# Optimization experiments

Measured on AMD Instinct MI355X. Metric: run time of the kernel, lower is better.

The kernel has to match this reference:

```python
import jax, jax.numpy as jnp
import numpy as np

R_SOFTPLUS_0 = 1.442695041  # 1/softplus(0) = 1/ln(2)
NEG_INF = -1e9


def setup_inputs() -> dict:
    key = jax.random.key(0)
    ks = jax.random.split(key, 6)
    B, L, E, H = 16, 1024, 512, 8
    Dh = E // H
    return {
        "x": jax.random.normal(ks[0], (B, L, E), jnp.float32),
        "in_proj_weight": jax.random.normal(ks[1], (3 * E, E), jnp.float32) * (E ** -0.5),
        "in_proj_bias": jax.random.normal(ks[2], (3 * E,), jnp.float32) * 0.02,
        "out_proj_weight": jax.random.normal(ks[3], (E, E), jnp.float32) * (E ** -0.5),
        "out_proj_bias": jax.random.normal(ks[4], (E,), jnp.float32) * 0.02,
        "qs_scale": jnp.zeros((Dh,), jnp.float32),  # init.zeros in QueryScaler
        "key_padding_mask": jnp.zeros((B, L), jnp.bool_),  # True = ignore key
    }


def reference(x, in_proj_weight, in_proj_bias, out_proj_weight, out_proj_bias,
              qs_scale, key_padding_mask):
    B, L, E = x.shape
    Dh = qs_scale.shape[0]
    H = E // Dh
    # packed in-projection: q,k,v = x @ W^T + b, split along last dim
    qkv = jnp.einsum("ble,fe->blf", x, in_proj_weight) + in_proj_bias
    q, k, v = jnp.split(qkv, 3, axis=-1)
    q = q.reshape(B, L, H, Dh)
    k = k.reshape(B, L, H, Dh)
    v = v.reshape(B, L, H, Dh)
    # QueryScaler: per-head-dim learned softplus scale on projected q
    q = q * (R_SOFTPLUS_0 * jax.nn.softplus(qs_scale))
    # scaled dot-product attention
    scores = jnp.einsum("blhd,bshd->bhls", q, k) / jnp.sqrt(jnp.asarray(Dh, q.dtype))
    scores = jnp.where(key_padding_mask[:, None, None, :], NEG_INF, scores)
    probs = jax.nn.softmax(scores, axis=-1)
    out = jnp.einsum("bhls,bshd->blhd", probs, v).reshape(B, L, E)
    # output projection
    return jnp.einsum("ble,fe->blf", out, out_proj_weight) + out_proj_bias
```

## Files before the change

### kernel.cpp

```cpp
#include <hip/hip_runtime.h>
#include <hip/hip_bf16.h>
#include <math.h>

#define B_ 16
#define L_ 1024
#define E_ 512
#define H_ 8
#define DH 64

typedef unsigned short u16;
typedef __attribute__((ext_vector_type(8))) short bf16x8;
typedef __attribute__((ext_vector_type(8))) unsigned short u16x8;
typedef __attribute__((ext_vector_type(4))) float f32x4;
typedef __attribute__((ext_vector_type(16))) float f32x16;

#define MFMA16(A, B, C) __builtin_amdgcn_mfma_f32_16x16x32_bf16(A, B, C, 0, 0, 0)
#define MFMA32(A, B, C) __builtin_amdgcn_mfma_f32_32x32x16_bf16(A, B, C, 0, 0, 0)

#if __has_builtin(__builtin_amdgcn_exp2f)
#define EXP2(x) __builtin_amdgcn_exp2f(x)
#else
#define EXP2(x) exp2f(x)
#endif

__device__ inline u16 f2b(float x) {
    __hip_bfloat16 h = __float2bfloat16(x);
    u16 u; __builtin_memcpy(&u, &h, 2); return u;
}

__device__ inline unsigned int cvt_pk_bf16(float a, float b) {
    unsigned int r;
    asm("v_cvt_pk_bf16_f32 %0, %1, %2" : "=v"(r) : "v"(a), "v"(b));
    return r;
}

__global__ void qscale_kernel(const float* __restrict__ qs_scale,
                              float* __restrict__ qscale) {
    int d = threadIdx.x;
    if (d < DH) {
        float x = qs_scale[d];
        float sp = (x > 20.f) ? x : log1pf(expf(x));
        qscale[d] = 1.442695041f * sp * 0.125f * 1.442695041f;
    }
}

__global__ __launch_bounds__(256) void cvt_bf16(
    const float* __restrict__ x, const float* __restrict__ wi,
    const float* __restrict__ wo, u16* __restrict__ xb,
    u16* __restrict__ wib, u16* __restrict__ wob)
{
    int i = blockIdx.x * 256 + threadIdx.x;
    const float* src; u16* dst; size_t off;
    if (i < 1048576)      { src = x;  dst = xb;  off = (size_t)i * 8; }
    else if (i < 1146880) { src = wi; dst = wib; off = (size_t)(i - 1048576) * 8; }
    else                  { src = wo; dst = wob; off = (size_t)(i - 1146880) * 8; }
    float4 a = *(const float4*)(src + off);
    float4 b = *(const float4*)(src + off + 4);
    u16x8 r;
    r[0] = f2b(a.x); r[1] = f2b(a.y); r[2] = f2b(a.z); r[3] = f2b(a.w);
    r[4] = f2b(b.x); r[5] = f2b(b.y); r[6] = f2b(b.z); r[7] = f2b(b.w);
    *(u16x8*)(dst + off) = r;
}

template<int MODE>
__global__ __launch_bounds__(256) void gemm_bf16(
    const u16* __restrict__ A, const u16* __restrict__ W,
    const float* __restrict__ bias, const float* __restrict__ qscale,
    float* __restrict__ Dout, u16* __restrict__ Qb, u16* __restrict__ Kb,
    u16* __restrict__ Vtb)
{
    __shared__ u16 sA[128][36];
    __shared__ u16 sB[128][36];
    const int tid = threadIdx.x;
    const int m0 = blockIdx.x * 128;
    const int n0 = blockIdx.y * 128;
    const int wid = tid >> 6, lane = tid & 63;
    const int g = lane >> 4, c = lane & 15;
    const int wr = wid >> 1, wc = wid & 1;

    const int srow = tid >> 2;
    const int sslot = tid & 3;
    const u16* Ap = A + (size_t)(m0 + srow) * 512 + sslot * 8;
    const u16* Wp = W + (size_t)(n0 + srow) * 512 + sslot * 8;

    f32x4 acc[4][4];
    #pragma unroll
    for (int m = 0; m < 4; m++)
        #pragma unroll
        for (int n = 0; n < 4; n++) acc[m][n] = (f32x4){0.f, 0.f, 0.f, 0.f};

    bf16x8 ra0 = *(const bf16x8*)(Ap);
    bf16x8 ra1 = *(const bf16x8*)(Ap + (size_t)64 * 512);
    bf16x8 rb0 = *(const bf16x8*)(Wp);
    bf16x8 rb1 = *(const bf16x8*)(Wp + (size_t)64 * 512);

    #pragma unroll 1
    for (int ks = 0; ks < 16; ks++) {
        __syncthreads();
        *(bf16x8*)&sA[srow][sslot * 8] = ra0;
        *(bf16x8*)&sA[srow + 64][sslot * 8] = ra1;
        *(bf16x8*)&sB[srow][sslot * 8] = rb0;
        *(bf16x8*)&sB[srow + 64][sslot * 8] = rb1;
        __syncthreads();
        if (ks < 15) {
            int k0 = (ks + 1) * 32;
            ra0 = *(const bf16x8*)(Ap + k0);
            ra1 = *(const bf16x8*)(Ap + (size_t)64 * 512 + k0);
            rb0 = *(const bf16x8*)(Wp + k0);
            rb1 = *(const bf16x8*)(Wp + (size_t)64 * 512 + k0);
        }
        bf16x8 af[4], bfr[4];
        #pragma unroll
        for (int m = 0; m < 4; m++)
            af[m] = *(const bf16x8*)&sA[wr * 64 + m * 16 + c][g * 8];
        #pragma unroll
        for (int n = 0; n < 4; n++)
            bfr[n] = *(const bf16x8*)&sB[wc * 64 + n * 16 + c][g * 8];
        #pragma unroll
        for (int m = 0; m < 4; m++)
            #pragma unroll
            for (int n = 0; n < 4; n++)
                acc[m][n] = MFMA16(af[m], bfr[n], acc[m][n]);
    }

    #pragma unroll
    for (int m = 0; m < 4; m++) {
        int rbase = m0 + wr * 64 + m * 16 + 4 * g;
        #pragma unroll
        for (int n = 0; n < 4; n++) {
            int f = n0 + wc * 64 + n * 16 + c;
            f32x4 v = acc[m][n];
            float bv = bias[f];
            if (MODE == 1) {
                #pragma unroll
                for (int reg = 0; reg < 4; reg++)
                    Dout[(size_t)(rbase + reg) * E_ + f] = v[reg] + bv;
            } else {
                int part = f >> 9, w = f & 511, h = w >> 6, d = w & 63;
                int bb = rbase >> 10;
                int l0 = rbase & 1023;
                size_t bh = (size_t)(bb * H_ + h);
                if (part == 0) {
                    float qs = qscale[d];
                    #pragma unroll
                    for (int reg = 0; reg < 4; reg++)
                        Qb[(bh * L_ + l0 + reg) * DH + d] = f2b((v[reg] + bv) * qs);
                } else if (part == 1) {
                    #pragma unroll
                    for (int reg = 0; reg < 4; reg++)
                        Kb[(bh * L_ + l0 + reg) * DH + d] = f2b(v[reg] + bv);
                } else {
                    ushort4 pk;
                    pk.x = f2b(v[0] + bv); pk.y = f2b(v[1] + bv);
                    pk.z = f2b(v[2] + bv); pk.w = f2b(v[3] + bv);
                    *(ushort4*)(Vtb + (bh * DH + d) * L_ + l0) = pk;
                }
            }
        }
    }
}

__global__ __launch_bounds__(256, 4) void attn_mfma(
    const u16* __restrict__ Q, const u16* __restrict__ K,
    const u16* __restrict__ Vt, const unsigned char* __restrict__ mask,
    u16* __restrict__ O)
{
    __shared__ u16 Kbuf[2][2048];
    __shared__ u16 Vbuf[2][2048];
    __shared__ u16 P_lds[4][32][36];

    const int bid = blockIdx.x;
    const int w = (bid & 7) * 128 + (bid >> 3);
    const int bh = w >> 3;
    const int blk = w & 7;
    const int tid = threadIdx.x;
    const int wid = tid >> 6;
    const int q0 = blk * 128 + wid * 32;
    const int b = bh >> 3;
    const int h = bh & (H_ - 1);

    const int lane = tid & 63;
    const int c = lane & 31;
    const int hi = lane >> 5;

    const u16* Qp = Q + ((size_t)bh * L_ + q0) * DH;
    const u16* Kp = K + (size_t)bh * L_ * DH;
    const u16* Vp = Vt + (size_t)bh * DH * L_;
    const unsigned char* mp = mask + (size_t)b * L_;

    const int krow = tid >> 3, kch = (tid & 7) ^ (krow & 7);
    const int vrow = tid >> 2, vch = (tid & 3) ^ ((vrow & 3) ^ ((vrow >> 2) & 3));
    const u16* Kg = Kp + (size_t)krow * DH + kch * 8;
    const u16* Vg = Vp + (size_t)vrow * L_ + vch * 8;

    auto stage = [&](int nbuf, int kt) {
        __builtin_amdgcn_global_load_lds(
            (const __attribute__((address_space(1))) unsigned int*)(Kg + (size_t)kt * DH),
            (__attribute__((address_space(3))) unsigned int*)&Kbuf[nbuf][wid * 512],
            16, 0, 0);
        __builtin_amdgcn_global_load_lds(
            (const __attribute__((address_space(1))) unsigned int*)(Vg + kt),
            (__attribute__((address_space(3))) unsigned int*)&Vbuf[nbuf][wid * 512],
            16, 0, 0);
    };

    unsigned int mor = 0;
    {
        const unsigned int* mp32 = (const unsigned int*)mp;
        #pragma unroll
        for (int i = 0; i < 4; i++) mor |= mp32[lane + i * 64];
    }
    const bool anyMask = (__ballot(mor != 0) != 0ULL);

    stage(0, 0);

    bf16x8 qf[4];
    #pragma unroll
    for (int s2 = 0; s2 < 4; s2++)
        qf[s2] = *(const bf16x8*)(Qp + c * DH + s2 * 16 + hi * 8);

    f32x16 oacc0 = {}, oacc1 = {};
    float mrun = -INFINITY, lrun = 0.f;

    int kslot[4];
    #pragma unroll
    for (int s2 = 0; s2 < 4; s2++)
        kslot[s2] = (c * 8 + (((2 * s2 + hi)) ^ (c & 7))) * 8;
    const int swzv = (c & 3) ^ ((c >> 2) & 3);
    int vslot[2][2];
    #pragma unroll
    for (int dt = 0; dt < 2; dt++)
        #pragma unroll
        for (int s = 0; s < 2; s++)
            vslot[dt][s] = ((dt * 32 + c) * 4 + (((2 * s + hi)) ^ swzv)) * 8;

    #pragma unroll 1
    for (int t = 0; t < 32; ++t) {
        const int cur = t & 1;
        const int kt = t * 32;
        asm volatile("s_waitcnt vmcnt(0) lgkmcnt(0)" ::: "memory");
        __syncthreads();

        bf16x8 kf[4];
        #pragma unroll
        for (int s2 = 0; s2 < 4; s2++)
            kf[s2] = *(const bf16x8*)&Kbuf[cur][kslot[s2]];
        bf16x8 vf[2][2];
        #pragma unroll
        for (int dt = 0; dt < 2; dt++)
            #pragma unroll
            for (int s = 0; s < 2; s++)
                vf[dt][s] = *(const bf16x8*)&Vbuf[cur][vslot[dt][s]];

        if (t < 31) stage(cur ^ 1, kt + 32);

        f32x16 st = {};
        #pragma unroll
        for (int s2 = 0; s2 < 4; s2++)
            st = MFMA32(kf[s2], qf[s2], st);

        if (anyMask) {
            #pragma unroll
            for (int r = 0; r < 16; r++) {
                int key = kt + (r & 3) + 8 * (r >> 2) + 4 * hi;
                if (mp[key]) st[r] = -1e9f;
            }
        }

        float m01 = fmaxf(st[0], st[1]),  m23 = fmaxf(st[2], st[3]);
        float m45 = fmaxf(st[4], st[5]),  m67 = fmaxf(st[6], st[7]);
        float m89 = fmaxf(st[8], st[9]),  mab = fmaxf(st[10], st[11]);
        float mcd = fmaxf(st[12], st[13]), mef = fmaxf(st[14], st[15]);
        float tm = fmaxf(fmaxf(fmaxf(m01, m23), fmaxf(m45, m67)),
                         fmaxf(fmaxf(m89, mab), fmaxf(mcd, mef)));
        tm = fmaxf(tm, __shfl_xor(tm, 32));

        if (!__all(tm <= mrun + 8.f)) {
            float mnew = fmaxf(mrun, tm);
            float corr = EXP2(mrun - mnew);
            lrun *= corr;
            #pragma unroll
            for (int r = 0; r < 16; r++) {
                int row = (r & 3) + 8 * (r >> 2) + 4 * hi;
                float cr = __shfl(corr, row);
                oacc0[r] *= cr;
                oacc1[r] *= cr;
            }
            mrun = mnew;
        }

        float p[16];
        #pragma unroll
        for (int r = 0; r < 16; r++) p[r] = EXP2(st[r] - mrun);
        float s01 = (p[0] + p[1]) + (p[2] + p[3]);
        float s23 = (p[4] + p[5]) + (p[6] + p[7]);
        float s45 = (p[8] + p[9]) + (p[10] + p[11]);
        float s67 = (p[12] + p[13]) + (p[14] + p[15]);
        float ls = (s01 + s23) + (s45 + s67);
        ls += __shfl_xor(ls, 32);
        lrun += ls;

        #pragma unroll
        for (int rp = 0; rp < 4; rp++) {
            uint2 pw;
            pw.x = cvt_pk_bf16(p[4 * rp], p[4 * rp + 1]);
            pw.y = cvt_pk_bf16(p[4 * rp + 2], p[4 * rp + 3]);
            *(uint2*)(&P_lds[wid][c][8 * rp + 4 * hi]) = pw;
        }
        asm volatile("s_waitcnt lgkmcnt(0)" ::: "memory");
        __builtin_amdgcn_sched_barrier(0);
        bf16x8 pa0 = *(const bf16x8*)(&P_lds[wid][c][hi * 8]);
        bf16x8 pa1 = *(const bf16x8*)(&P_lds[wid][c][16 + hi * 8]);
        asm volatile("" ::: "memory");

        oacc0 = MFMA32(pa0, vf[0][0], oacc0);
        oacc0 = MFMA32(pa1, vf[0][1], oacc0);
        oacc1 = MFMA32(pa0, vf[1][0], oacc1);
        oacc1 = MFMA32(pa1, vf[1][1], oacc1);
    }

    #pragma unroll
    for (int r = 0; r < 16; r++) {
        int row = (r & 3) + 8 * (r >> 2) + 4 * hi;
        float lq = __shfl(lrun, row);
        float inv = 1.f / lq;
        size_t base = ((size_t)(b * L_ + q0 + row)) * E_ + h * DH + c;
        O[base] = f2b(oacc0[r] * inv);
        O[base + 32] = f2b(oacc1[r] * inv);
    }
}

extern "C" void kernel_launch(void* const* d_in, const int* in_sizes, int n_in,
                              void* d_out, int out_size, void* d_ws, size_t ws_size,
                              hipStream_t stream) {
    const float* x     = (const float*)d_in[0];
    const float* w_in  = (const float*)d_in[1];
    const float* b_in  = (const float*)d_in[2];
    const float* w_out = (const float*)d_in[3];
    const float* b_out = (const float*)d_in[4];
    const float* qs    = (const float*)d_in[5];
    const unsigned char* mask = (const unsigned char*)d_in[6];
    float* out = (float*)d_out;

    char* base = (char*)d_ws;
    const size_t NELEM = (size_t)B_ * L_ * E_;
    float* qscale = (float*)base;
    u16* xb  = (u16*)(base + 256);
    u16* wib = xb + NELEM;
    u16* wob = wib + 786432;
    u16* Qb  = wob + 262144;
    u16* Kb  = Qb + NELEM;
    u16* Vtb = Kb + NELEM;
    u16* Ob  = Vtb + NELEM;

    qscale_kernel<<<1, 64, 0, stream>>>(qs, qscale);
    cvt_bf16<<<4608, 256, 0, stream>>>(x, w_in, w_out, xb, wib, wob);
    gemm_bf16<0><<<dim3(128, 12), 256, 0, stream>>>(
        xb, wib, b_in, qscale, nullptr, Qb, Kb, Vtb);
    attn_mfma<<<dim3(1024), 256, 0, stream>>>(Qb, Kb, Vtb, mask, Ob);
    gemm_bf16<1><<<dim3(128, 4), 256, 0, stream>>>(
        Ob, wob, b_out, nullptr, out, nullptr, nullptr, nullptr);
}
```

Baseline: 130.0 us.

## Use direct global-to-LDS loads with double-buffered swizzled tiles in GEMM

Replaces the register-staged global loads plus LDS stores in the bf16 GEMM with global_load_lds builtins that write straight into a double-buffered shared-memory tile. The layout drops the padded rows for an XOR-swizzled 32-element row layout, meant to avoid LDS bank conflicts on the MFMA fragment reads. The loop now needs a single barrier per k-step, and the next tile's load overlaps the current MFMAs. This doubles LDS use, and the explicit vmcnt(0) wait serializes on the prefetch each iteration.

Result: no change. 130.4 us (+0.3%).

```diff
diff --git a/kernel.cpp b/kernel.cpp
--- a/kernel.cpp
+++ b/kernel.cpp
@@ -69,8 +69,8 @@
     float* __restrict__ Dout, u16* __restrict__ Qb, u16* __restrict__ Kb,
     u16* __restrict__ Vtb)
 {
-    __shared__ u16 sA[128][36];
-    __shared__ u16 sB[128][36];
+    __shared__ u16 sA[2][4096];
+    __shared__ u16 sB[2][4096];
     const int tid = threadIdx.x;
     const int m0 = blockIdx.x * 128;
     const int n0 = blockIdx.y * 128;
@@ -78,10 +78,27 @@
     const int g = lane >> 4, c = lane & 15;
     const int wr = wid >> 1, wc = wid & 1;
 
-    const int srow = tid >> 2;
-    const int sslot = tid & 3;
-    const u16* Ap = A + (size_t)(m0 + srow) * 512 + sslot * 8;
-    const u16* Wp = W + (size_t)(n0 + srow) * 512 + sslot * 8;
+    const int arow = tid >> 2;
+    const int swg = (arow & 3) ^ ((arow >> 2) & 3);
+    const int ch = (tid & 3) ^ swg;
+    const u16* Asrc = A + (size_t)(m0 + arow) * 512 + ch * 8;
+    const u16* Bsrc = W + (size_t)(n0 + arow) * 512 + ch * 8;
+
+    auto stage = [&](int nbuf, int ks) {
+        const int k0 = ks * 32;
+        __builtin_amdgcn_global_load_lds(
+            (const __attribute__((address_space(1))) unsigned int*)(Asrc + k0),
+            (__attribute__((address_space(3))) unsigned int*)&sA[nbuf][wid * 512], 16, 0, 0);
+        __builtin_amdgcn_global_load_lds(
+            (const __attribute__((address_space(1))) unsigned int*)(Asrc + (size_t)64 * 512 + k0),
+            (__attribute__((address_space(3))) unsigned int*)&sA[nbuf][2048 + wid * 512], 16, 0, 0);
+        __builtin_amdgcn_global_load_lds(
+            (const __attribute__((address_space(1))) unsigned int*)(Bsrc + k0),
+            (__attribute__((address_space(3))) unsigned int*)&sB[nbuf][wid * 512], 16, 0, 0);
+        __builtin_amdgcn_global_load_lds(
+            (const __attribute__((address_space(1))) unsigned int*)(Bsrc + (size_t)64 * 512 + k0),
+            (__attribute__((address_space(3))) unsigned int*)&sB[nbuf][2048 + wid * 512], 16, 0, 0);
+    };
 
     f32x4 acc[4][4];
     #pragma unroll
@@ -89,33 +106,24 @@
         #pragma unroll
         for (int n = 0; n < 4; n++) acc[m][n] = (f32x4){0.f, 0.f, 0.f, 0.f};
 
-    bf16x8 ra0 = *(const bf16x8*)(Ap);
-    bf16x8 ra1 = *(const bf16x8*)(Ap + (size_t)64 * 512);
-    bf16x8 rb0 = *(const bf16x8*)(Wp);
-    bf16x8 rb1 = *(const bf16x8*)(Wp + (size_t)64 * 512);
-
+    const int swr = (c & 3) ^ ((c >> 2) & 3);
+    const int chA = (g ^ swr) * 8;
+
+    stage(0, 0);
     #pragma unroll 1
     for (int ks = 0; ks < 16; ks++) {
+        const int cur = ks & 1;
+        asm volatile("s_waitcnt vmcnt(0) lgkmcnt(0)" ::: "memory");
         __syncthreads();
-        *(bf16x8*)&sA[srow][sslot * 8] = ra0;
-        *(bf16x8*)&sA[srow + 64][sslot * 8] = ra1;
-        *(bf16x8*)&sB[srow][sslot * 8] = rb0;
-        *(bf16x8*)&sB[srow + 64][sslot * 8] = rb1;
-        __syncthreads();
-        if (ks < 15) {
-            int k0 = (ks + 1) * 32;
-            ra0 = *(const bf16x8*)(Ap + k0);
-            ra1 = *(const bf16x8*)(Ap + (size_t)64 * 512 + k0);
-            rb0 = *(const bf16x8*)(Wp + k0);
-            rb1 = *(const bf16x8*)(Wp + (size_t)64 * 512 + k0);
-        }
+        if (ks < 15) stage(cur ^ 1, ks + 1);
+
         bf16x8 af[4], bfr[4];
         #pragma unroll
         for (int m = 0; m < 4; m++)
-            af[m] = *(const bf16x8*)&sA[wr * 64 + m * 16 + c][g * 8];
+            af[m] = *(const bf16x8*)&sA[cur][(wr * 64 + m * 16 + c) * 32 + chA];
         #pragma unroll
         for (int n = 0; n < 4; n++)
-            bfr[n] = *(const bf16x8*)&sB[wc * 64 + n * 16 + c][g * 8];
+            bfr[n] = *(const bf16x8*)&sB[cur][(wc * 64 + n * 16 + c) * 32 + chA];
         #pragma unroll
         for (int m = 0; m < 4; m++)
             #pragma unroll
```
